# Performance work log

Measured on AMD Instinct MI355X. Metric: run time of the kernel, lower is better.

## Reference

```python
import jax, jax.numpy as jnp
import numpy as np

TEMPERATURE = 0.5


def _nt_xent(emb_i, emb_j, temperature):
    n = emb_i.shape[0]
    reps = jnp.concatenate([emb_i, emb_j], axis=0)  # [2N, D]
    # cosine similarity via normalized GEMM (same math as broadcasted F.cosine_similarity)
    eps = 1e-8
    norms = jnp.maximum(jnp.linalg.norm(reps, axis=1, keepdims=True), eps)
    z = reps / norms
    sim = z @ z.T  # [2N, 2N]
    # positives: sim[k, k+N] for k<N and sim[k, k-N] for k>=N
    sim_ij = jnp.diagonal(sim, offset=n)
    sim_ji = jnp.diagonal(sim, offset=-n)
    positives = jnp.concatenate([sim_ij, sim_ji], axis=0)  # [2N]
    logits = sim / temperature
    # mask out self-similarity (diagonal) in denominator
    neg_mask = 1.0 - jnp.eye(2 * n, dtype=logits.dtype)
    denom = jnp.sum(neg_mask * jnp.exp(logits), axis=1)  # [2N]
    loss_partial = -(positives / temperature - jnp.log(denom))
    return jnp.sum(loss_partial) / (2 * n)


def setup_inputs() -> dict:
    key = jax.random.key(0)
    k1, k2 = jax.random.split(key)
    N, D = 4096, 256
    emb_i = jax.random.normal(k1, (N, D), dtype=jnp.float32)
    emb_j = jax.random.normal(k2, (N, D), dtype=jnp.float32)
    return {"emb_i": emb_i, "emb_j": emb_j}


def reference(emb_i, emb_j):
    return _nt_xent(emb_i, emb_j, TEMPERATURE)
```

## Files before the change

### kernel.cpp

```cpp
#include <hip/hip_runtime.h>
#include <hip/hip_bf16.h>
#include <math.h>

#define D      256
#define N2     8192
#define NHALF  4096
#define TILE   128
#define BK     64
#define NCH    4
#define LDW    68
#define NBLK2  4096
#define TPB    512

typedef __bf16 bf16x8_t __attribute__((ext_vector_type(8)));
typedef __bf16 bf16x4_t __attribute__((ext_vector_type(4)));
typedef float  f32x4_t  __attribute__((ext_vector_type(4)));

__global__ __launch_bounds__(256) void prep_kernel(const float* __restrict__ a,
                                                   const float* __restrict__ b,
                                                   __bf16* __restrict__ zb,
                                                   float* __restrict__ g_pos,
                                                   float* __restrict__ g_denom,
                                                   unsigned* __restrict__ g_t1) {
    const int tid = threadIdx.x;
    const int gt  = blockIdx.x * 256 + tid;
    if (gt < N2) g_denom[gt] = 0.0f;
    if (gt < 64 * 32 + 1) g_t1[gt] = 0u;

    const int w = blockIdx.x * 4 + (tid >> 6);
    const int l = tid & 63;
    float4 x = ((const float4*)(a + (size_t)w * D))[l];
    float4 y = ((const float4*)(b + (size_t)w * D))[l];
    float sxx = x.x * x.x + x.y * x.y + x.z * x.z + x.w * x.w;
    float syy = y.x * y.y * 0.0f + y.x * y.x + y.y * y.y + y.z * y.z + y.w * y.w;
    float sxy = x.x * y.x + x.y * y.y + x.z * y.z + x.w * y.w;
    #pragma unroll
    for (int off = 32; off; off >>= 1) {
        sxx += __shfl_xor(sxx, off, 64);
        syy += __shfl_xor(syy, off, 64);
        sxy += __shfl_xor(sxy, off, 64);
    }
    const float rx = 1.0f / fmaxf(sqrtf(sxx), 1e-8f);
    const float ry = 1.0f / fmaxf(sqrtf(syy), 1e-8f);

    bf16x4_t ox, oy;
    ox[0] = (__bf16)(x.x * rx); ox[1] = (__bf16)(x.y * rx);
    ox[2] = (__bf16)(x.z * rx); ox[3] = (__bf16)(x.w * rx);
    oy[0] = (__bf16)(y.x * ry); oy[1] = (__bf16)(y.y * ry);
    oy[2] = (__bf16)(y.z * ry); oy[3] = (__bf16)(y.w * ry);
    *(bf16x4_t*)(zb + (size_t)w * D + l * 4)           = ox;
    *(bf16x4_t*)(zb + (size_t)(w + NHALF) * D + l * 4) = oy;

    if (l == 0) {
        const float p = sxy * rx * ry;
        g_pos[w]         = p;
        g_pos[w + NHALF] = p;
    }
}

__global__ __launch_bounds__(TPB, 4) void sim_kernel(const __bf16* __restrict__ zb,
                                                     float* __restrict__ g_denom,
                                                     const float* __restrict__ g_pos,
                                                     unsigned* __restrict__ g_t1,
                                                     float* __restrict__ out) {
    __shared__ __bf16 ldsA[2][TILE * LDW];
    __shared__ __bf16 ldsB[2][TILE * LDW];
    __shared__ float  sw[8];
    __shared__ bool   amLast;

    const int tid    = threadIdx.x;
    const int l      = tid & 63;
    const int lane15 = l & 15;
    const int quad   = l >> 4;
    const int w      = tid >> 6;
    const int wr     = (w & 3) * 32;
    const int wc     = (w >> 2) * 64;

    const int bi = blockIdx.x >> 6;
    const int bj = blockIdx.x & 63;

    const int r = tid >> 2;
    const int u = tid & 3;
    const __bf16* ga = zb + (size_t)(bi * TILE + r) * D + u * 8;
    const __bf16* gb = zb + (size_t)(bj * TILE + r) * D + u * 8;
    const int wofs = r * LDW + u * 8;

    bf16x8_t sa0, sa1, sb0, sb1;
    auto load_regs = [&](int c) {
        const int k0 = c * BK;
        sa0 = *(const bf16x8_t*)(ga + k0);
        sa1 = *(const bf16x8_t*)(ga + k0 + 32);
        sb0 = *(const bf16x8_t*)(gb + k0);
        sb1 = *(const bf16x8_t*)(gb + k0 + 32);
    };
    auto write_lds = [&](int buf) {
        *(bf16x8_t*)(&ldsA[buf][wofs])      = sa0;
        *(bf16x8_t*)(&ldsA[buf][wofs + 32]) = sa1;
        *(bf16x8_t*)(&ldsB[buf][wofs])      = sb0;
        *(bf16x8_t*)(&ldsB[buf][wofs + 32]) = sb1;
    };

    f32x4_t acc[2][4];
    #pragma unroll
    for (int mi = 0; mi < 2; ++mi)
        #pragma unroll
        for (int nj = 0; nj < 4; ++nj)
            acc[mi][nj] = (f32x4_t){0.f, 0.f, 0.f, 0.f};

    auto compute = [&](int buf) {
        #pragma unroll
        for (int ks = 0; ks < 2; ++ks) {
            bf16x8_t af[2], bff[4];
            #pragma unroll
            for (int mi = 0; mi < 2; ++mi)
                af[mi] = *(const bf16x8_t*)(&ldsA[buf][(wr + mi * 16 + lane15) * LDW + ks * 32 + quad * 8]);
            #pragma unroll
            for (int nj = 0; nj < 4; ++nj)
                bff[nj] = *(const bf16x8_t*)(&ldsB[buf][(wc + nj * 16 + lane15) * LDW + ks * 32 + quad * 8]);
            #pragma unroll
            for (int mi = 0; mi < 2; ++mi)
                #pragma unroll
                for (int nj = 0; nj < 4; ++nj)
                    acc[mi][nj] = __builtin_amdgcn_mfma_f32_16x16x32_bf16(bff[nj], af[mi], acc[mi][nj], 0, 0, 0);
        }
    };

    load_regs(0);
    write_lds(0);
    __syncthreads();

    int cur = 0;
    #pragma unroll
    for (int c = 0; c < NCH; ++c) {
        if (c + 1 < NCH) load_regs(c + 1);
        compute(cur);
        if (c + 1 < NCH) {
            write_lds(cur ^ 1);
            __syncthreads();
            cur ^= 1;
        }
    }

    float rs[2] = {0.f, 0.f};
    #pragma unroll
    for (int mi = 0; mi < 2; ++mi) {
        #pragma unroll
        for (int nj = 0; nj < 4; ++nj) {
            const bool dn = (bi == bj) && (wr + mi * 16 == wc + nj * 16);
            #pragma unroll
            for (int t = 0; t < 4; ++t) {
                float e = exp2f(acc[mi][nj][t] * 2.8853900817779268f);
                if (dn && (quad * 4 + t) == lane15) e = 0.0f;
                rs[mi] += e;
            }
        }
    }
    #pragma unroll
    for (int mi = 0; mi < 2; ++mi) {
        rs[mi] += __shfl_xor(rs[mi], 16, 64);
        rs[mi] += __shfl_xor(rs[mi], 32, 64);
    }
    if (l < 16) {
        #pragma unroll
        for (int mi = 0; mi < 2; ++mi)
            atomicAdd(&g_denom[bi * TILE + wr + mi * 16 + l], rs[mi]);
    }

    __syncthreads();
    if (tid == 0) {
        asm volatile("s_waitcnt vmcnt(0)" ::: "memory");
        unsigned t1 = __hip_atomic_fetch_add(&g_t1[bi * 32], 1u, __ATOMIC_RELAXED,
                                             __HIP_MEMORY_SCOPE_AGENT);
        bool grpLast = (t1 == 63);
        unsigned t2 = 0;
        if (grpLast)
            t2 = __hip_atomic_fetch_add(&g_t1[64 * 32], 1u, __ATOMIC_RELAXED,
                                        __HIP_MEMORY_SCOPE_AGENT);
        amLast = grpLast && (t2 == 63);
    }
    __syncthreads();
    if (!amLast) return;

    float local = 0.0f;
    for (int k = tid; k < N2; k += TPB) {
        float dn = __hip_atomic_load(&g_denom[k], __ATOMIC_RELAXED,
                                     __HIP_MEMORY_SCOPE_AGENT);
        local += logf(dn) - 2.0f * g_pos[k];
    }
    #pragma unroll
    for (int off = 32; off; off >>= 1) local += __shfl_xor(local, off, 64);
    if (l == 0) sw[w] = local;
    __syncthreads();
    if (tid == 0) {
        float s = 0.f;
        #pragma unroll
        for (int i = 0; i < 8; ++i) s += sw[i];
        out[0] = s / (float)N2;
    }
}

extern "C" void kernel_launch(void* const* d_in, const int* in_sizes, int n_in,
                              void* d_out, int out_size, void* d_ws, size_t ws_size,
                              hipStream_t stream) {
    const float* emb_i = (const float*)d_in[0];
    const float* emb_j = (const float*)d_in[1];

    __bf16*   zb      = (__bf16*)d_ws;
    float*    g_denom = (float*)((char*)d_ws + (size_t)N2 * D * 2);
    float*    g_pos   = g_denom + N2;
    unsigned* g_t1    = (unsigned*)(g_pos + N2);
    float*    out     = (float*)d_out;

    prep_kernel<<<NHALF / 4, 256, 0, stream>>>(emb_i, emb_j, zb, g_pos, g_denom, g_t1);
    sim_kernel<<<NBLK2, TPB, 0, stream>>>(zb, g_denom, g_pos, g_t1, out);
}
```

Measured before the change: 122.4 us.

## Fuse normalization into similarity GEMM by scaling raw dot products

Drops the separate prep kernel that normalized rows and wrote a bf16 copy. The GEMM now loads raw fp32 inputs, converts them to bf16 while staging into LDS, and accumulates squared norms along the way. It then scales the raw dot products by the reciprocal norms before the exp, and the diagonal blocks write the positive similarities. This removes one launch and the bf16 intermediate round trip. In exchange each tile reads fp32 (twice the global traffic, with heavy re-reading across 4096 blocks), adds a hipMemsetAsync, and rounds unnormalized values to bf16.

```diff
diff --git a/kernel.cpp b/kernel.cpp
--- a/kernel.cpp
+++ b/kernel.cpp
@@ -13,58 +13,15 @@
 #define TPB    512
 
 typedef __bf16 bf16x8_t __attribute__((ext_vector_type(8)));
-typedef __bf16 bf16x4_t __attribute__((ext_vector_type(4)));
 typedef float  f32x4_t  __attribute__((ext_vector_type(4)));
 
-__global__ __launch_bounds__(256) void prep_kernel(const float* __restrict__ a,
-                                                   const float* __restrict__ b,
-                                                   __bf16* __restrict__ zb,
-                                                   float* __restrict__ g_pos,
-                                                   float* __restrict__ g_denom,
-                                                   unsigned* __restrict__ g_t1) {
-    const int tid = threadIdx.x;
-    const int gt  = blockIdx.x * 256 + tid;
-    if (gt < N2) g_denom[gt] = 0.0f;
-    if (gt < 64 * 32 + 1) g_t1[gt] = 0u;
-
-    const int w = blockIdx.x * 4 + (tid >> 6);
-    const int l = tid & 63;
-    float4 x = ((const float4*)(a + (size_t)w * D))[l];
-    float4 y = ((const float4*)(b + (size_t)w * D))[l];
-    float sxx = x.x * x.x + x.y * x.y + x.z * x.z + x.w * x.w;
-    float syy = y.x * y.y * 0.0f + y.x * y.x + y.y * y.y + y.z * y.z + y.w * y.w;
-    float sxy = x.x * y.x + x.y * y.y + x.z * y.z + x.w * y.w;
-    #pragma unroll
-    for (int off = 32; off; off >>= 1) {
-        sxx += __shfl_xor(sxx, off, 64);
-        syy += __shfl_xor(syy, off, 64);
-        sxy += __shfl_xor(sxy, off, 64);
-    }
-    const float rx = 1.0f / fmaxf(sqrtf(sxx), 1e-8f);
-    const float ry = 1.0f / fmaxf(sqrtf(syy), 1e-8f);
-
-    bf16x4_t ox, oy;
-    ox[0] = (__bf16)(x.x * rx); ox[1] = (__bf16)(x.y * rx);
-    ox[2] = (__bf16)(x.z * rx); ox[3] = (__bf16)(x.w * rx);
-    oy[0] = (__bf16)(y.x * ry); oy[1] = (__bf16)(y.y * ry);
-    oy[2] = (__bf16)(y.z * ry); oy[3] = (__bf16)(y.w * ry);
-    *(bf16x4_t*)(zb + (size_t)w * D + l * 4)           = ox;
-    *(bf16x4_t*)(zb + (size_t)(w + NHALF) * D + l * 4) = oy;
-
-    if (l == 0) {
-        const float p = sxy * rx * ry;
-        g_pos[w]         = p;
-        g_pos[w + NHALF] = p;
-    }
-}
-
-__global__ __launch_bounds__(TPB, 4) void sim_kernel(const __bf16* __restrict__ zb,
-                                                     float* __restrict__ g_denom,
-                                                     const float* __restrict__ g_pos,
-                                                     unsigned* __restrict__ g_t1,
-                                                     float* __restrict__ out) {
+__global__ __launch_bounds__(TPB, 4) void fused_kernel(
+        const float* __restrict__ a, const float* __restrict__ b,
+        float* __restrict__ g_denom, float* __restrict__ g_pos,
+        unsigned* __restrict__ g_t1, float* __restrict__ out) {
     __shared__ __bf16 ldsA[2][TILE * LDW];
     __shared__ __bf16 ldsB[2][TILE * LDW];
+    __shared__ float  rnA[TILE], rnB[TILE];
     __shared__ float  sw[8];
     __shared__ bool   amLast;
 
@@ -79,25 +36,43 @@
     const int bi = blockIdx.x >> 6;
     const int bj = blockIdx.x & 63;
 
+    const float* pa = (bi < 32) ? (a + (size_t)bi * TILE * D)
+                                : (b + (size_t)(bi - 32) * TILE * D);
+    const float* pb = (bj < 32) ? (a + (size_t)bj * TILE * D)
+                                : (b + (size_t)(bj - 32) * TILE * D);
+
     const int r = tid >> 2;
-    const int u = tid & 3;
-    const __bf16* ga = zb + (size_t)(bi * TILE + r) * D + u * 8;
-    const __bf16* gb = zb + (size_t)(bj * TILE + r) * D + u * 8;
-    const int wofs = r * LDW + u * 8;
-
-    bf16x8_t sa0, sa1, sb0, sb1;
+    const int q = tid & 3;
+    const float* gar = pa + (size_t)r * D + q * 16;
+    const float* gbr = pb + (size_t)r * D + q * 16;
+    const int wofs = r * LDW + q * 16;
+
+    float ssa = 0.f, ssb = 0.f;
+    f32x4_t va[4], vb[4];
     auto load_regs = [&](int c) {
-        const int k0 = c * BK;
-        sa0 = *(const bf16x8_t*)(ga + k0);
-        sa1 = *(const bf16x8_t*)(ga + k0 + 32);
-        sb0 = *(const bf16x8_t*)(gb + k0);
-        sb1 = *(const bf16x8_t*)(gb + k0 + 32);
+        const float* A0 = gar + c * BK;
+        const float* B0 = gbr + c * BK;
+        #pragma unroll
+        for (int u = 0; u < 4; ++u) {
+            va[u] = *(const f32x4_t*)(A0 + u * 4);
+            vb[u] = *(const f32x4_t*)(B0 + u * 4);
+        }
     };
     auto write_lds = [&](int buf) {
-        *(bf16x8_t*)(&ldsA[buf][wofs])      = sa0;
-        *(bf16x8_t*)(&ldsA[buf][wofs + 32]) = sa1;
-        *(bf16x8_t*)(&ldsB[buf][wofs])      = sb0;
-        *(bf16x8_t*)(&ldsB[buf][wofs + 32]) = sb1;
+        bf16x8_t oa0, oa1, ob0, ob1;
+        #pragma unroll
+        for (int e = 0; e < 4; ++e) {
+            oa0[e]     = (__bf16)va[0][e]; oa0[e + 4] = (__bf16)va[1][e];
+            oa1[e]     = (__bf16)va[2][e]; oa1[e + 4] = (__bf16)va[3][e];
+            ob0[e]     = (__bf16)vb[0][e]; ob0[e + 4] = (__bf16)vb[1][e];
+            ob1[e]     = (__bf16)vb[2][e]; ob1[e + 4] = (__bf16)vb[3][e];
+            ssa += va[0][e]*va[0][e] + va[1][e]*va[1][e] + va[2][e]*va[2][e] + va[3][e]*va[3][e];
+            ssb += vb[0][e]*vb[0][e] + vb[1][e]*vb[1][e] + vb[2][e]*vb[2][e] + vb[3][e]*vb[3][e];
+        }
+        *(bf16x8_t*)(&ldsA[buf][wofs])     = oa0;
+        *(bf16x8_t*)(&ldsA[buf][wofs + 8]) = oa1;
+        *(bf16x8_t*)(&ldsB[buf][wofs])     = ob0;
+        *(bf16x8_t*)(&ldsB[buf][wofs + 8]) = ob1;
     };
 
     f32x4_t acc[2][4];
@@ -141,16 +116,39 @@
         }
     }
 
+    ssa += __shfl_xor(ssa, 1, 64); ssa += __shfl_xor(ssa, 2, 64);
+    ssb += __shfl_xor(ssb, 1, 64); ssb += __shfl_xor(ssb, 2, 64);
+    if (q == 0) {
+        rnA[r] = 1.0f / fmaxf(sqrtf(ssa), 1e-8f);
+        rnB[r] = 1.0f / fmaxf(sqrtf(ssb), 1e-8f);
+    }
+    __syncthreads();
+
+    float rsA[2], rsB4[4][4];
+    #pragma unroll
+    for (int mi = 0; mi < 2; ++mi) rsA[mi] = rnA[wr + mi * 16 + lane15];
+    #pragma unroll
+    for (int nj = 0; nj < 4; ++nj)
+        #pragma unroll
+        for (int t = 0; t < 4; ++t) rsB4[nj][t] = rnB[wc + nj * 16 + quad * 4 + t];
+
+    const bool posBlk = (bj == bi + 32);
     float rs[2] = {0.f, 0.f};
     #pragma unroll
     for (int mi = 0; mi < 2; ++mi) {
         #pragma unroll
         for (int nj = 0; nj < 4; ++nj) {
-            const bool dn = (bi == bj) && (wr + mi * 16 == wc + nj * 16);
+            const bool dg = (wr + mi * 16 == wc + nj * 16);
             #pragma unroll
             for (int t = 0; t < 4; ++t) {
-                float e = exp2f(acc[mi][nj][t] * 2.8853900817779268f);
-                if (dn && (quad * 4 + t) == lane15) e = 0.0f;
+                const float s = acc[mi][nj][t] * rsA[mi] * rsB4[nj][t];
+                float e = exp2f(s * 2.8853900817779268f);
+                if (dg && (quad * 4 + t) == lane15) {
+                    if (bi == bj) e = 0.0f;
+                    if (posBlk)
+                        __hip_atomic_store(&g_pos[bi * TILE + wr + mi * 16 + lane15], s,
+                                           __ATOMIC_RELAXED, __HIP_MEMORY_SCOPE_AGENT);
+                }
                 rs[mi] += e;
             }
         }
@@ -185,7 +183,12 @@
     for (int k = tid; k < N2; k += TPB) {
         float dn = __hip_atomic_load(&g_denom[k], __ATOMIC_RELAXED,
                                      __HIP_MEMORY_SCOPE_AGENT);
-        local += logf(dn) - 2.0f * g_pos[k];
+        local += logf(dn);
+        if (k < NHALF) {
+            float p = __hip_atomic_load(&g_pos[k], __ATOMIC_RELAXED,
+                                        __HIP_MEMORY_SCOPE_AGENT);
+            local -= 4.0f * p;
+        }
     }
     #pragma unroll
     for (int off = 32; off; off >>= 1) local += __shfl_xor(local, off, 64);
@@ -205,12 +208,11 @@
     const float* emb_i = (const float*)d_in[0];
     const float* emb_j = (const float*)d_in[1];
 
-    __bf16*   zb      = (__bf16*)d_ws;
-    float*    g_denom = (float*)((char*)d_ws + (size_t)N2 * D * 2);
-    float*    g_pos   = g_denom + N2;
-    unsigned* g_t1    = (unsigned*)(g_pos + N2);
+    float*    g_denom = (float*)d_ws;
+    unsigned* g_t1    = (unsigned*)(g_denom + N2);
+    float*    g_pos   = (float*)(g_t1 + 64 * 32 + 8);
     float*    out     = (float*)d_out;
 
-    prep_kernel<<<NHALF / 4, 256, 0, stream>>>(emb_i, emb_j, zb, g_pos, g_denom, g_t1);
-    sim_kernel<<<NBLK2, TPB, 0, stream>>>(zb, g_denom, g_pos, g_t1, out);
+    hipMemsetAsync(d_ws, 0, (size_t)N2 * 4 + (64 * 32 + 8) * 4, stream);
+    fused_kernel<<<NBLK2, TPB, 0, stream>>>(emb_i, emb_j, g_denom, g_pos, g_t1, out);
 }
```

New measurement: 164.1 us. 34.1% more time.
